# Optimization experiments

Hardware: AMD Instinct MI355X
Metric: run time of the kernel (lower is better)

Reference implementation:

```python
import jax, jax.numpy as jnp
import numpy as np

HEADS = 16

def _binarize(W):
    # alpha: per-output-row mean of |W| (reduce over all dims except dim 0)
    alpha = jnp.mean(jnp.abs(W), axis=tuple(range(1, W.ndim)), keepdims=True)
    # straight-through sign: forward sign(W), backward identity
    B = W + jax.lax.stop_gradient(jnp.sign(W) - W)
    return alpha * B

def _binlinear(x, W, b):
    Wb = _binarize(W)
    return jnp.einsum('btc,oc->bto', x, Wb) + b

def setup_inputs() -> dict:
    key = jax.random.key(0)
    ks = jax.random.split(key, 9)
    dim = 1024
    B, T = 4, 2048
    inp = {
        'x': jax.random.normal(ks[0], (B, T, dim), jnp.float32),
        'Wq': jax.random.normal(ks[1], (dim, dim), jnp.float32) * 0.02,
        'bq': jax.random.normal(ks[2], (dim,), jnp.float32) * 0.02,
        'Wk': jax.random.normal(ks[3], (dim, dim), jnp.float32) * 0.02,
        'bk': jax.random.normal(ks[4], (dim,), jnp.float32) * 0.02,
        'Wv': jax.random.normal(ks[5], (dim, dim), jnp.float32) * 0.02,
        'bv': jax.random.normal(ks[6], (dim,), jnp.float32) * 0.02,
        'Wp': jax.random.normal(ks[7], (dim, dim), jnp.float32) * 0.02,
        'bp': jax.random.normal(ks[8], (dim,), jnp.float32) * 0.02,
    }
    return inp

def reference(x, Wq, bq, Wk, bk, Wv, bv, Wp, bp):
    B, T, C = x.shape
    H = HEADS
    Dh = C // H
    scale = Dh ** -0.5

    def split_heads(t):
        return t.reshape(B, T, H, Dh).transpose(0, 2, 1, 3)  # [B,H,T,Dh]

    q = split_heads(_binlinear(x, Wq, bq))
    k = split_heads(_binlinear(x, Wk, bk))
    v = split_heads(_binlinear(x, Wv, bv))

    att = jnp.einsum('bhtd,bhsd->bhts', q, k) * scale  # [B,H,T,T]
    att = jax.nn.softmax(att, axis=-1)
    y = jnp.einsum('bhts,bhsd->bhtd', att, v)  # [B,H,T,Dh]
    y = y.transpose(0, 2, 1, 3).reshape(B, T, C)
    return _binlinear(y, Wp, bp)
```

## Files before the change

### kernel.cpp

```cpp
#include <hip/hip_runtime.h>
#include <hip/hip_bf16.h>

typedef short s16x8 __attribute__((ext_vector_type(8)));
typedef float f32x4 __attribute__((ext_vector_type(4)));
typedef unsigned short u16;

#define LOG2E 1.4426950408889634f
#define QSC (0.125f * LOG2E)

typedef __attribute__((address_space(3))) unsigned int lds_u32;
typedef __attribute__((address_space(1))) const unsigned int glb_u32;

static __device__ __forceinline__ void gload16(const void* g, void* l) {
  __builtin_amdgcn_global_load_lds((glb_u32*)g, (lds_u32*)l, 16, 0, 0);
}
static __device__ __forceinline__ u16 bf16u(float f) {
  unsigned u = __builtin_bit_cast(unsigned, f);
  return (u16)((u + 0x7FFFu + ((u >> 16) & 1u)) >> 16);
}
static __device__ __forceinline__ unsigned pk(u16 a, u16 b) {
  return (unsigned)a | ((unsigned)b << 16);
}
static __device__ __forceinline__ unsigned pk2(float a, float b) {
  float2 f; f.x = a; f.y = b;
  __hip_bfloat162 h = __float22bfloat162_rn(f);
  unsigned r;
  __builtin_memcpy(&r, &h, 4);
  return r;
}

__global__ __launch_bounds__(256) void k_prep(
    const float* __restrict__ x, u16* __restrict__ xb,
    const float* __restrict__ Wq, const float* __restrict__ Wk,
    const float* __restrict__ Wv, const float* __restrict__ Wp,
    const float* __restrict__ bq, const float* __restrict__ bk,
    const float* __restrict__ bv, const float* __restrict__ bp,
    u16* __restrict__ wbqkv, u16* __restrict__ wbp,
    float* __restrict__ alphaf, float* __restrict__ biasf) {
  if (blockIdx.x >= 1024) {
    int i = ((blockIdx.x - 1024) * 256 + threadIdx.x) * 8;
    float4 a = *reinterpret_cast<const float4*>(x + i);
    float4 b = *reinterpret_cast<const float4*>(x + i + 4);
    uint4 w = { pk2(a.x, a.y), pk2(a.z, a.w), pk2(b.x, b.y), pk2(b.z, b.w) };
    *reinterpret_cast<uint4*>(xb + i) = w;
    return;
  }
  int wave = threadIdx.x >> 6, lane = threadIdx.x & 63;
  int row = blockIdx.x * 4 + wave;
  const float* src; const float* bias; int r;
  if (row < 1024)      { src = Wq; bias = bq; r = row; }
  else if (row < 2048) { src = Wk; bias = bk; r = row - 1024; }
  else if (row < 3072) { src = Wv; bias = bv; r = row - 2048; }
  else                 { src = Wp; bias = bp; r = row - 3072; }
  const float4* s4 = reinterpret_cast<const float4*>(src + r * 1024);
  float4 v[4];
  float asum = 0.f;
#pragma unroll
  for (int i = 0; i < 4; ++i) {
    v[i] = s4[lane * 4 + i];
    asum += fabsf(v[i].x) + fabsf(v[i].y) + fabsf(v[i].z) + fabsf(v[i].w);
  }
#pragma unroll
  for (int m = 32; m >= 1; m >>= 1) asum += __shfl_xor(asum, m, 64);
  float alpha = asum * (1.0f / 1024.0f);

  u16 o[16];
#pragma unroll
  for (int i = 0; i < 4; ++i) {
    const float* f = reinterpret_cast<const float*>(&v[i]);
#pragma unroll
    for (int j = 0; j < 4; ++j) {
      float w = f[j];
      o[i * 4 + j] = (w > 0.f) ? (u16)0x3F80 : ((w < 0.f) ? (u16)0xBF80 : (u16)0);
    }
  }
  u16* dst = (row < 3072 ? wbqkv + row * 1024 : wbp + (row - 3072) * 1024) + lane * 16;
  uint4 w0 = { pk(o[0],o[1]), pk(o[2],o[3]), pk(o[4],o[5]), pk(o[6],o[7]) };
  uint4 w1 = { pk(o[8],o[9]), pk(o[10],o[11]), pk(o[12],o[13]), pk(o[14],o[15]) };
  reinterpret_cast<uint4*>(dst)[0] = w0;
  reinterpret_cast<uint4*>(dst)[1] = w1;
  if (lane == 0) {
    float sc = (row < 1024) ? QSC : 1.0f;
    alphaf[row] = alpha * sc;
    biasf[row]  = bias[r] * sc;
  }
}

template <int MODE, int NX, int NWG>
__global__ __launch_bounds__(256) void k_gemm(
    const u16* __restrict__ A, const u16* __restrict__ Bw,
    const float* __restrict__ alphaf, const float* __restrict__ biasf,
    u16* __restrict__ qbuf, u16* __restrict__ kbuf, u16* __restrict__ vtbuf,
    float* __restrict__ outf) {
  __shared__ alignas(128) char smem[33792];
  char* As = smem;
  char* Bs = smem + 16384;
  int tid = threadIdx.x;
  int wave = tid >> 6, l = tid & 63, g = l >> 4, ln = l & 15;
  int wm = (wave >> 1) * 64, wn = (wave & 1) * 64;
  int wg = (blockIdx.x & 7) * (NWG / 8) + (blockIdx.x >> 3);
  int m0 = (wg / NX) * 128, n0 = (wg % NX) * 128;

  f32x4 acc[4][4];
#pragma unroll
  for (int i = 0; i < 4; ++i)
#pragma unroll
    for (int j = 0; j < 4; ++j) acc[i][j] = f32x4{0.f, 0.f, 0.f, 0.f};

  const char* Ab = reinterpret_cast<const char*>(A) + m0 * 2048;
  const char* Bb = reinterpret_cast<const char*>(Bw) + n0 * 2048;

  int soff[4];
#pragma unroll
  for (int i = 0; i < 4; ++i) {
    int P = i * 4096 + tid * 16;
    int r = P >> 7;
    int kc = ((P >> 4) & 7) ^ (r & 7);
    soff[i] = r * 2048 + kc * 16;
  }

  for (int ks = 0; ks < 16; ++ks) {
    int kb0 = ks * 128;
#pragma unroll
    for (int i = 0; i < 4; ++i)
      gload16(Ab + soff[i] + kb0, As + i * 4096 + wave * 1024);
#pragma unroll
    for (int i = 0; i < 4; ++i)
      gload16(Bb + soff[i] + kb0, Bs + i * 4096 + wave * 1024);
    __syncthreads();
#pragma unroll
    for (int kk = 0; kk < 2; ++kk) {
      s16x8 af[4], bfr[4];
#pragma unroll
      for (int mf = 0; mf < 4; ++mf) {
        int r = wm + mf * 16 + ln;
        int kb = (kk * 64 + g * 16) ^ ((r & 7) << 4);
        af[mf] = *reinterpret_cast<const s16x8*>(As + r * 128 + kb);
      }
#pragma unroll
      for (int nf = 0; nf < 4; ++nf) {
        int r = wn + nf * 16 + ln;
        int kb = (kk * 64 + g * 16) ^ ((r & 7) << 4);
        bfr[nf] = *reinterpret_cast<const s16x8*>(Bs + r * 128 + kb);
      }
#pragma unroll
      for (int mf = 0; mf < 4; ++mf)
#pragma unroll
        for (int nf = 0; nf < 4; ++nf)
          acc[mf][nf] = __builtin_amdgcn_mfma_f32_16x16x32_bf16(af[mf], bfr[nf], acc[mf][nf], 0, 0, 0);
    }
    __syncthreads();
  }

  if (MODE == 0) {
    if (n0 < 2048) {
      u16* dst = (n0 < 1024) ? qbuf : kbuf;
#pragma unroll
      for (int nf = 0; nf < 4; ++nf) {
        int n = n0 + wn + nf * 16 + ln;
        float al = alphaf[n], bi = biasf[n];
        int nl = n & 1023;
        int h = nl >> 6, d = nl & 63;
#pragma unroll
        for (int mf = 0; mf < 4; ++mf)
#pragma unroll
          for (int rg = 0; rg < 4; ++rg) {
            int m = m0 + wm + mf * 16 + g * 4 + rg;
            int b = m >> 11, t = m & 2047;
            dst[(((b * 16 + h) * 2048 + t) << 6) + d] = bf16u(al * acc[mf][nf][rg] + bi);
          }
      }
    } else {
      u16* ldsT = reinterpret_cast<u16*>(smem);
#pragma unroll
      for (int nf = 0; nf < 4; ++nf) {
        int n = n0 + wn + nf * 16 + ln;
        float al = alphaf[n], bi = biasf[n];
        int nloc = wn + nf * 16 + ln;
#pragma unroll
        for (int mf = 0; mf < 4; ++mf)
#pragma unroll
          for (int rg = 0; rg < 4; ++rg) {
            int mloc = wm + mf * 16 + g * 4 + rg;
            ldsT[mloc * 132 + nloc] = bf16u(al * acc[mf][nf][rg] + bi);
          }
      }
      __syncthreads();
      int dl = tid >> 1;
      int sh = (tid & 1) * 64;
      int nv = n0 - 2048 + dl;
      int h = nv >> 6, d = nv & 63;
      int b = m0 >> 11;
      int s0 = (m0 & 2047) + sh;
      u16* vdst = vtbuf + (((b * 16 + h) * 64 + d) << 11) + s0;
#pragma unroll
      for (int c8 = 0; c8 < 8; ++c8) {
        u16 t0 = ldsT[(sh + c8 * 8 + 0) * 132 + dl], t1 = ldsT[(sh + c8 * 8 + 1) * 132 + dl];
        u16 t2 = ldsT[(sh + c8 * 8 + 2) * 132 + dl], t3 = ldsT[(sh + c8 * 8 + 3) * 132 + dl];
        u16 t4 = ldsT[(sh + c8 * 8 + 4) * 132 + dl], t5 = ldsT[(sh + c8 * 8 + 5) * 132 + dl];
        u16 t6 = ldsT[(sh + c8 * 8 + 6) * 132 + dl], t7 = ldsT[(sh + c8 * 8 + 7) * 132 + dl];
        uint4 w = { pk(t0, t1), pk(t2, t3), pk(t4, t5), pk(t6, t7) };
        *reinterpret_cast<uint4*>(vdst + c8 * 8) = w;
      }
    }
  } else {
#pragma unroll
    for (int nf = 0; nf < 4; ++nf) {
      int n = n0 + wn + nf * 16 + ln;
      float al = alphaf[3072 + n], bi = biasf[3072 + n];
#pragma unroll
      for (int mf = 0; mf < 4; ++mf)
#pragma unroll
        for (int rg = 0; rg < 4; ++rg) {
          int m = m0 + wm + mf * 16 + g * 4 + rg;
          outf[m * 1024 + n] = al * acc[mf][nf][rg] + bi;
        }
    }
  }
}

__global__ __launch_bounds__(512, 4) void k_attn(
    const u16* __restrict__ qb, const u16* __restrict__ kb,
    const u16* __restrict__ vtb, u16* __restrict__ yb) {
  __shared__ alignas(128) char smem[65536];
  int tid = threadIdx.x;
  int wave = tid >> 6, lane = tid & 63;
  int g = lane >> 4, ln = lane & 15;
  int swz = (ln & 7) << 4;

  int wg = (blockIdx.x & 7) * 64 + (blockIdx.x >> 3);
  int bh = wg >> 3, qt = wg & 7;
  const char* Qg = reinterpret_cast<const char*>(qb) + bh * 262144;
  const char* Kg = reinterpret_cast<const char*>(kb) + bh * 262144;
  const char* Vg = reinterpret_cast<const char*>(vtb) + bh * 262144;

  int qrow = qt * 256 + wave * 32 + ln;
  const s16x8* Qr0 = reinterpret_cast<const s16x8*>(Qg + qrow * 128);
  const s16x8* Qr1 = reinterpret_cast<const s16x8*>(Qg + (qrow + 16) * 128);
  s16x8 qf[2][2];
  qf[0][0] = Qr0[g]; qf[0][1] = Qr0[g + 4];
  qf[1][0] = Qr1[g]; qf[1][1] = Qr1[g + 4];

  s16x8 ones;
#pragma unroll
  for (int i = 0; i < 8; ++i) ones[i] = (short)0x3F80;

  int r = tid >> 3, kc = tid & 7;
  int swsrc = (kc ^ (r & 7)) * 16;
  int ksrc = r * 128 + swsrc;
  int vsrc = r * 4096 + swsrc;

  char* Ps = smem + 32768 + wave * 4096;

  f32x4 oacc[2][4];
#pragma unroll
  for (int s = 0; s < 2; ++s)
#pragma unroll
    for (int i = 0; i < 4; ++i) oacc[s][i] = f32x4{0.f, 0.f, 0.f, 0.f};
  f32x4 lacc[2];
  lacc[0] = f32x4{0.f, 0.f, 0.f, 0.f};
  lacc[1] = f32x4{0.f, 0.f, 0.f, 0.f};

  gload16(Kg + ksrc, smem + wave * 1024);
  gload16(Vg + vsrc, smem + 8192 + wave * 1024);
  __syncthreads();

  for (int st = 0; st < 32; ++st) {
    int cb = st & 1;
    if (st < 31) {
      int sb = (st + 1) * 64;
      char* nb = smem + (cb ^ 1) * 16384;
      gload16(Kg + sb * 128 + ksrc, nb + wave * 1024);
      gload16(Vg + sb * 2 + vsrc, nb + 8192 + wave * 1024);
    }
    const char* Kb = smem + cb * 16384;
    const char* Vb = Kb + 8192;

    f32x4 sacc[2][4];
#pragma unroll
    for (int s = 0; s < 2; ++s)
#pragma unroll
      for (int t = 0; t < 4; ++t) sacc[s][t] = f32x4{0.f, 0.f, 0.f, 0.f};
    __builtin_amdgcn_s_setprio(1);
#pragma unroll
    for (int kt = 0; kt < 2; ++kt) {
      int off = (kt * 64 + g * 16) ^ swz;
#pragma unroll
      for (int t = 0; t < 4; ++t) {
        s16x8 kf = *reinterpret_cast<const s16x8*>(Kb + (t * 16 + ln) * 128 + off);
        sacc[0][t] = __builtin_amdgcn_mfma_f32_16x16x32_bf16(kf, qf[0][kt], sacc[0][t], 0, 0, 0);
        sacc[1][t] = __builtin_amdgcn_mfma_f32_16x16x32_bf16(kf, qf[1][kt], sacc[1][t], 0, 0, 0);
      }
    }
    __builtin_amdgcn_s_setprio(0);

    s16x8 vfr[2][4];
#pragma unroll
    for (int kt = 0; kt < 2; ++kt) {
      int off = (kt * 64 + g * 16) ^ swz;
#pragma unroll
      for (int dt = 0; dt < 4; ++dt)
        vfr[kt][dt] = *reinterpret_cast<const s16x8*>(Vb + (dt * 16 + ln) * 128 + off);
    }

#pragma unroll
    for (int s = 0; s < 2; ++s) {
      char* Pr = Ps + (s * 16 + ln) * 128;
#pragma unroll
      for (int t = 0; t < 4; ++t) {
        float e0 = __builtin_amdgcn_exp2f(sacc[s][t][0]);
        float e1 = __builtin_amdgcn_exp2f(sacc[s][t][1]);
        float e2 = __builtin_amdgcn_exp2f(sacc[s][t][2]);
        float e3 = __builtin_amdgcn_exp2f(sacc[s][t][3]);
        uint2 w;
        w.x = pk2(e0, e1);
        w.y = pk2(e2, e3);
        *reinterpret_cast<uint2*>(Pr + ((t * 32 + g * 8) ^ swz)) = w;
      }
    }

    s16x8 pf[2][2];
#pragma unroll
    for (int s = 0; s < 2; ++s) {
      const char* Pr = Ps + (s * 16 + ln) * 128;
      pf[s][0] = *reinterpret_cast<const s16x8*>(Pr + ((g * 16) ^ swz));
      pf[s][1] = *reinterpret_cast<const s16x8*>(Pr + ((64 + g * 16) ^ swz));
    }

#pragma unroll
    for (int s = 0; s < 2; ++s)
#pragma unroll
      for (int kt = 0; kt < 2; ++kt)
        lacc[s] = __builtin_amdgcn_mfma_f32_16x16x32_bf16(ones, pf[s][kt], lacc[s], 0, 0, 0);

    __builtin_amdgcn_s_setprio(1);
#pragma unroll
    for (int kt = 0; kt < 2; ++kt) {
#pragma unroll
      for (int dt = 0; dt < 4; ++dt) {
        oacc[0][dt] = __builtin_amdgcn_mfma_f32_16x16x32_bf16(vfr[kt][dt], pf[0][kt], oacc[0][dt], 0, 0, 0);
        oacc[1][dt] = __builtin_amdgcn_mfma_f32_16x16x32_bf16(vfr[kt][dt], pf[1][kt], oacc[1][dt], 0, 0, 0);
      }
    }
    __builtin_amdgcn_s_setprio(0);
    __syncthreads();
  }

  int b = bh >> 4, h = bh & 15;
#pragma unroll
  for (int s = 0; s < 2; ++s) {
    float linv = 1.0f / lacc[s][0];
    u16* yrow = yb + (b * 2048 + qrow + s * 16) * 1024 + h * 64;
#pragma unroll
    for (int dt = 0; dt < 4; ++dt) {
      uint2 w;
      w.x = pk2(oacc[s][dt][0] * linv, oacc[s][dt][1] * linv);
      w.y = pk2(oacc[s][dt][2] * linv, oacc[s][dt][3] * linv);
      *reinterpret_cast<uint2*>(yrow + dt * 16 + g * 4) = w;
    }
  }
}

extern "C" void kernel_launch(void* const* d_in, const int* in_sizes, int n_in,
                              void* d_out, int out_size, void* d_ws, size_t ws_size,
                              hipStream_t stream) {
  (void)in_sizes; (void)n_in; (void)out_size; (void)ws_size;
  const float* x  = (const float*)d_in[0];
  const float* Wq = (const float*)d_in[1];
  const float* bq = (const float*)d_in[2];
  const float* Wk = (const float*)d_in[3];
  const float* bk = (const float*)d_in[4];
  const float* Wv = (const float*)d_in[5];
  const float* bv = (const float*)d_in[6];
  const float* Wp = (const float*)d_in[7];
  const float* bp = (const float*)d_in[8];

  char* ws = (char*)d_ws;
  u16*   xb    = (u16*)(ws);
  u16*   wbqkv = (u16*)(ws + 16777216);
  u16*   wbp   = (u16*)(ws + 23068672);
  float* alphaf = (float*)(ws + 25165824);
  float* biasf  = (float*)(ws + 25182208);
  u16*   vtbuf = (u16*)(ws + 25198592);
  u16*   ybuf  = xb;
  u16*   qbuf  = (u16*)d_out;
  u16*   kbuf  = (u16*)d_out + 8388608;
  float* outf  = (float*)d_out;

  k_prep<<<5120, 256, 0, stream>>>(x, xb, Wq, Wk, Wv, Wp, bq, bk, bv, bp, wbqkv, wbp, alphaf, biasf);
  k_gemm<0, 24, 1536><<<1536, 256, 0, stream>>>(xb, wbqkv, alphaf, biasf, qbuf, kbuf, vtbuf, nullptr);
  k_attn<<<512, 512, 0, stream>>>(qbuf, kbuf, vtbuf, ybuf);
  k_gemm<1, 8, 512><<<512, 256, 0, stream>>>(ybuf, wbp, alphaf, biasf, nullptr, nullptr, nullptr, outf);
}
```

Measured before the change: 174.5 us.

## Keep attention probabilities in registers via permuted K row order

```diff
diff --git a/kernel.cpp b/kernel.cpp
--- a/kernel.cpp
+++ b/kernel.cpp
@@ -3,6 +3,7 @@
 
 typedef short s16x8 __attribute__((ext_vector_type(8)));
 typedef float f32x4 __attribute__((ext_vector_type(4)));
+typedef unsigned u32x4 __attribute__((ext_vector_type(4)));
 typedef unsigned short u16;
 
 #define LOG2E 1.4426950408889634f
@@ -222,11 +223,10 @@
 __global__ __launch_bounds__(512, 4) void k_attn(
     const u16* __restrict__ qb, const u16* __restrict__ kb,
     const u16* __restrict__ vtb, u16* __restrict__ yb) {
-  __shared__ alignas(128) char smem[65536];
+  __shared__ alignas(128) char smem[32768];
   int tid = threadIdx.x;
   int wave = tid >> 6, lane = tid & 63;
   int g = lane >> 4, ln = lane & 15;
-  int swz = (ln & 7) << 4;
 
   int wg = (blockIdx.x & 7) * 64 + (blockIdx.x >> 3);
   int bh = wg >> 3, qt = wg & 7;
@@ -246,11 +246,13 @@
   for (int i = 0; i < 8; ++i) ones[i] = (short)0x3F80;
 
   int r = tid >> 3, kc = tid & 7;
-  int swsrc = (kc ^ (r & 7)) * 16;
+  int wr = (r & 3) | (((r >> 3) & 1) << 2);
+  int swsrc = (kc ^ wr) * 16;
   int ksrc = r * 128 + swsrc;
   int vsrc = r * 4096 + swsrc;
 
-  char* Ps = smem + 32768 + wave * 4096;
+  int swK = (ln & 7) << 4;
+  int swV = ((ln & 3) | (((ln >> 3) & 1) << 2)) << 4;
 
   f32x4 oacc[2][4];
 #pragma unroll
@@ -284,47 +286,35 @@
     __builtin_amdgcn_s_setprio(1);
 #pragma unroll
     for (int kt = 0; kt < 2; ++kt) {
-      int off = (kt * 64 + g * 16) ^ swz;
+      int off = (kt * 64 + g * 16) ^ swK;
 #pragma unroll
       for (int t = 0; t < 4; ++t) {
-        s16x8 kf = *reinterpret_cast<const s16x8*>(Kb + (t * 16 + ln) * 128 + off);
+        int rho = 32 * (t & 1) + 8 * (ln >> 2) + 4 * (t >> 1) + (ln & 3);
+        s16x8 kf = *reinterpret_cast<const s16x8*>(Kb + rho * 128 + off);
         sacc[0][t] = __builtin_amdgcn_mfma_f32_16x16x32_bf16(kf, qf[0][kt], sacc[0][t], 0, 0, 0);
         sacc[1][t] = __builtin_amdgcn_mfma_f32_16x16x32_bf16(kf, qf[1][kt], sacc[1][t], 0, 0, 0);
       }
     }
     __builtin_amdgcn_s_setprio(0);
 
-    s16x8 vfr[2][4];
-#pragma unroll
-    for (int kt = 0; kt < 2; ++kt) {
-      int off = (kt * 64 + g * 16) ^ swz;
-#pragma unroll
-      for (int dt = 0; dt < 4; ++dt)
-        vfr[kt][dt] = *reinterpret_cast<const s16x8*>(Vb + (dt * 16 + ln) * 128 + off);
-    }
-
+    s16x8 pf[2][2];
 #pragma unroll
     for (int s = 0; s < 2; ++s) {
-      char* Pr = Ps + (s * 16 + ln) * 128;
-#pragma unroll
-      for (int t = 0; t < 4; ++t) {
-        float e0 = __builtin_amdgcn_exp2f(sacc[s][t][0]);
-        float e1 = __builtin_amdgcn_exp2f(sacc[s][t][1]);
-        float e2 = __builtin_amdgcn_exp2f(sacc[s][t][2]);
-        float e3 = __builtin_amdgcn_exp2f(sacc[s][t][3]);
-        uint2 w;
-        w.x = pk2(e0, e1);
-        w.y = pk2(e2, e3);
-        *reinterpret_cast<uint2*>(Pr + ((t * 32 + g * 8) ^ swz)) = w;
-      }
-    }
-
-    s16x8 pf[2][2];
-#pragma unroll
-    for (int s = 0; s < 2; ++s) {
-      const char* Pr = Ps + (s * 16 + ln) * 128;
-      pf[s][0] = *reinterpret_cast<const s16x8*>(Pr + ((g * 16) ^ swz));
-      pf[s][1] = *reinterpret_cast<const s16x8*>(Pr + ((64 + g * 16) ^ swz));
+      float p[4][4];
+#pragma unroll
+      for (int t = 0; t < 4; ++t)
+#pragma unroll
+        for (int rg = 0; rg < 4; ++rg)
+          p[t][rg] = __builtin_amdgcn_exp2f(sacc[s][t][rg]);
+#pragma unroll
+      for (int kt = 0; kt < 2; ++kt) {
+        u32x4 tw;
+        tw[0] = pk2(p[kt][0],     p[kt][1]);
+        tw[1] = pk2(p[kt][2],     p[kt][3]);
+        tw[2] = pk2(p[kt + 2][0], p[kt + 2][1]);
+        tw[3] = pk2(p[kt + 2][2], p[kt + 2][3]);
+        pf[s][kt] = __builtin_bit_cast(s16x8, tw);
+      }
     }
 
 #pragma unroll
@@ -336,10 +326,12 @@
     __builtin_amdgcn_s_setprio(1);
 #pragma unroll
     for (int kt = 0; kt < 2; ++kt) {
+      int off = (kt * 64 + g * 16) ^ swV;
 #pragma unroll
       for (int dt = 0; dt < 4; ++dt) {
-        oacc[0][dt] = __builtin_amdgcn_mfma_f32_16x16x32_bf16(vfr[kt][dt], pf[0][kt], oacc[0][dt], 0, 0, 0);
-        oacc[1][dt] = __builtin_amdgcn_mfma_f32_16x16x32_bf16(vfr[kt][dt], pf[1][kt], oacc[1][dt], 0, 0, 0);
+        s16x8 vf = *reinterpret_cast<const s16x8*>(Vb + (dt * 16 + ln) * 128 + off);
+        oacc[0][dt] = __builtin_amdgcn_mfma_f32_16x16x32_bf16(vf, pf[0][kt], oacc[0][dt], 0, 0, 0);
+        oacc[1][dt] = __builtin_amdgcn_mfma_f32_16x16x32_bf16(vf, pf[1][kt], oacc[1][dt], 0, 0, 0);
       }
     }
     __builtin_amdgcn_s_setprio(0);
```

Result: no change. 171.9 us (-1.5%).
